# Performance work log

Hardware: AMD Instinct MI355X
Metric: run time of the kernel (lower is better)

## Reference

```python
import jax, jax.numpy as jnp
import numpy as np
import math

N_NODES = 50000
N_EDGES = 800000
IN_CH = 128
HID_CH = 16   # per-head channels of conv1
OUT_CH = 1    # per-head channels of conv2 (forced so Linear(heads,100) type-checks)
HEADS = 8


def _seg_softmax(scores, seg, n):
    # softmax over edges grouped by target node (variable-size neighborhoods)
    m = jax.ops.segment_max(scores, seg, num_segments=n)
    e = jnp.exp(scores - m[seg])
    s = jax.ops.segment_sum(e, seg, num_segments=n)
    return e / (s[seg] + 1e-16)


def _transformer_conv(x, edge_index, Wq, bq, Wk, bk, Wv, bv, Ws, bs, heads, ch):
    # PyG TransformerConv, concat=True, root_weight=True, beta=False
    n = x.shape[0]
    src, dst = edge_index[0], edge_index[1]
    q = (x @ Wq + bq).reshape(n, heads, ch)
    k = (x @ Wk + bk).reshape(n, heads, ch)
    v = (x @ Wv + bv).reshape(n, heads, ch)
    qi = q[dst]              # [E, H, C] gather at target
    kj = k[src]              # [E, H, C] gather at source
    vj = v[src]              # [E, H, C]
    alpha = jnp.einsum('ehc,ehc->eh', qi, kj) / math.sqrt(ch)  # [E, H]
    alpha = _seg_softmax(alpha, dst, n)
    agg = jax.ops.segment_sum(vj * alpha[:, :, None], dst, num_segments=n)
    out = agg.reshape(n, heads * ch)
    return out + x @ Ws + bs   # skip connection lin_skip(x)


def setup_inputs() -> dict:
    key = jax.random.key(0)
    ks = jax.random.split(key, 16)
    s = 0.05
    d1 = HEADS * HID_CH  # 128
    d2 = HEADS * OUT_CH  # 8
    inp = {
        'x': jax.random.normal(ks[0], (N_NODES, IN_CH), dtype=jnp.float32),
        'edge_index': jax.random.randint(ks[1], (2, N_EDGES), 0, N_NODES),
        # conv1 params
        'Wq1': jax.random.normal(ks[2], (IN_CH, d1), dtype=jnp.float32) * s,
        'bq1': jnp.zeros((d1,), jnp.float32),
        'Wk1': jax.random.normal(ks[3], (IN_CH, d1), dtype=jnp.float32) * s,
        'bk1': jnp.zeros((d1,), jnp.float32),
        'Wv1': jax.random.normal(ks[4], (IN_CH, d1), dtype=jnp.float32) * s,
        'bv1': jnp.zeros((d1,), jnp.float32),
        'Ws1': jax.random.normal(ks[5], (IN_CH, d1), dtype=jnp.float32) * s,
        'bs1': jnp.zeros((d1,), jnp.float32),
        # conv2 params (in = hidden*heads = 128)
        'Wq2': jax.random.normal(ks[6], (d1, d2), dtype=jnp.float32) * s,
        'bq2': jnp.zeros((d2,), jnp.float32),
        'Wk2': jax.random.normal(ks[7], (d1, d2), dtype=jnp.float32) * s,
        'bk2': jnp.zeros((d2,), jnp.float32),
        'Wv2': jax.random.normal(ks[8], (d1, d2), dtype=jnp.float32) * s,
        'bv2': jnp.zeros((d2,), jnp.float32),
        'Ws2': jax.random.normal(ks[9], (d1, d2), dtype=jnp.float32) * s,
        'bs2': jnp.zeros((d2,), jnp.float32),
        # final linear: heads -> 100
        'Wl': jax.random.normal(ks[10], (HEADS, 100), dtype=jnp.float32) * s,
        'bl': jnp.zeros((100,), jnp.float32),
    }
    return inp


def reference(x, edge_index, Wq1, bq1, Wk1, bk1, Wv1, bv1, Ws1, bs1,
              Wq2, bq2, Wk2, bk2, Wv2, bv2, Ws2, bs2, Wl, bl):
    h = _transformer_conv(x, edge_index, Wq1, bq1, Wk1, bk1, Wv1, bv1, Ws1, bs1, HEADS, HID_CH)
    h = _transformer_conv(h, edge_index, Wq2, bq2, Wk2, bk2, Wv2, bv2, Ws2, bs2, HEADS, OUT_CH)
    h = jax.nn.relu(h @ Wl + bl)   # dropout is identity in eval mode
    return jnp.mean(h, axis=0, keepdims=True)   # [1, 100]
```

## Files before the change

kernel.cpp:

```cpp
#include <hip/hip_runtime.h>
#include <hip/hip_bf16.h>
#include <cstdint>
#include <cstddef>


typedef _Float16 f16x8 __attribute__((ext_vector_type(8)));
typedef _Float16 f16x4 __attribute__((ext_vector_type(4)));
typedef _Float16 f16x2 __attribute__((ext_vector_type(2)));
typedef float    f32x4 __attribute__((ext_vector_type(4)));
typedef float    f32x2 __attribute__((ext_vector_type(2)));

#define SCAN_PAD 4096

__global__ __launch_bounds__(256) void pack_weights(
    const float* __restrict__ Wq1, const float* __restrict__ bq1,
    const float* __restrict__ Wk1, const float* __restrict__ bk1,
    const float* __restrict__ Wv1, const float* __restrict__ bv1,
    const float* __restrict__ Ws1, const float* __restrict__ bs1,
    const float* __restrict__ Wq2, const float* __restrict__ bq2,
    const float* __restrict__ Wk2, const float* __restrict__ bk2,
    const float* __restrict__ Wv2, const float* __restrict__ bv2,
    const float* __restrict__ Ws2, const float* __restrict__ bs2,
    _Float16* __restrict__ Wt1, float* __restrict__ b1,
    _Float16* __restrict__ Wt2, float* __restrict__ b2,
    int* __restrict__ counts, float* __restrict__ out, int n, int out_size)
{
    int i = blockIdx.x * 256 + threadIdx.x;
    if (i < n + SCAN_PAD) counts[i] = 0;
    if (i < out_size) out[i] = 0.f;
    if (i < 65536) {
        int j = i >> 7, k = i & 127;
        const float* W; int col; float sc = 1.f;
        if (j < 128)      { W = Wq1; col = j; sc = 0.25f; }
        else if (j < 384) { int t = j - 128, c = t >> 2, r = t & 3;
                            if (r < 2) { W = Wk1; col = 2 * c + r; }
                            else       { W = Wv1; col = 2 * c + r - 2; } }
        else              { W = Ws1; col = j - 384; }
        Wt1[i] = (_Float16)(W[k * 128 + col] * sc);
    } else if (i < 66048) {
        int j = i - 65536;
        const float* B; int col; float sc = 1.f;
        if (j < 128)      { B = bq1; col = j; sc = 0.25f; }
        else if (j < 384) { int t = j - 128, c = t >> 2, r = t & 3;
                            if (r < 2) { B = bk1; col = 2 * c + r; }
                            else       { B = bv1; col = 2 * c + r - 2; } }
        else              { B = bs1; col = j - 384; }
        b1[j] = B[col] * sc;
    } else if (i < 66048 + 4096) {
        int t = i - 66048;
        int j = t >> 7, k = t & 127;
        const float* W; int col;
        if (j < 8)       { W = Wq2; col = j; }
        else if (j < 24) { int u = j - 8; col = u >> 1; W = (u & 1) ? Wv2 : Wk2; }
        else             { W = Ws2; col = j - 24; }
        Wt2[t] = (_Float16)W[k * 8 + col];
    } else if (i < 66048 + 4096 + 32) {
        int j = i - (66048 + 4096);
        const float* B; int col;
        if (j < 8)       { B = bq2; col = j; }
        else if (j < 24) { int u = j - 8; col = u >> 1; B = (u & 1) ? bv2 : bk2; }
        else             { B = bs2; col = j - 24; }
        b2[j] = B[col];
    }
}

__global__ __launch_bounds__(256) void rank_edges(
    const int* __restrict__ ei, int* __restrict__ counts,
    unsigned short* __restrict__ rank, int E)
{
    int e0 = (blockIdx.x * 256 + threadIdx.x) * 4;
    if (e0 + 4 <= E) {
        int4 d4 = *(const int4*)&ei[E + e0];
        int r0 = atomicAdd(&counts[d4.x], 1);
        int r1 = atomicAdd(&counts[d4.y], 1);
        int r2 = atomicAdd(&counts[d4.z], 1);
        int r3 = atomicAdd(&counts[d4.w], 1);
        ushort4 rr = make_ushort4((unsigned short)r0, (unsigned short)r1,
                                  (unsigned short)r2, (unsigned short)r3);
        *(ushort4*)&rank[e0] = rr;
    } else {
        for (int e = e0; e < E; ++e)
            rank[e] = (unsigned short)atomicAdd(&counts[ei[E + e]], 1);
    }
}

__global__ __launch_bounds__(1024) void scan_all(
    const int* __restrict__ counts, int* __restrict__ indptr, int n, int E)
{
    int t = threadIdx.x, lane = t & 63;
    int lo = t * 52;
    int4 c[13];
    #pragma unroll
    for (int j = 0; j < 13; ++j) c[j] = *(const int4*)&counts[lo + j * 4];
    int s = 0;
    #pragma unroll
    for (int j = 0; j < 13; ++j) s += c[j].x + c[j].y + c[j].z + c[j].w;
    int x = s;
    #pragma unroll
    for (int off = 1; off < 64; off <<= 1) {
        int y = __shfl_up(x, off, 64);
        if (lane >= off) x += y;
    }
    __shared__ int ws[16];
    if (lane == 63) ws[t >> 6] = x;
    __syncthreads();
    int woff = 0;
    #pragma unroll
    for (int w = 0; w < 15; ++w) if (w < (t >> 6)) woff += ws[w];
    int run = woff + x - s;
    #pragma unroll
    for (int j = 0; j < 13; ++j) {
        int i = lo + j * 4;
        int4 v = c[j];
        int p0 = run, p1 = p0 + v.x, p2 = p1 + v.y, p3 = p2 + v.z;
        run = p3 + v.w;
        if (i + 3 < n) {
            *(int4*)&indptr[i] = make_int4(p0, p1, p2, p3);
        } else {
            if (i < n)     indptr[i]     = p0;
            if (i + 1 < n) indptr[i + 1] = p1;
            if (i + 2 < n) indptr[i + 2] = p2;
            if (i + 3 < n) indptr[i + 3] = p3;
        }
    }
    if (t == 0) indptr[n] = E;
}

__global__ __launch_bounds__(256) void place_edges(
    const int* __restrict__ ei, const int* __restrict__ indptr,
    const unsigned short* __restrict__ rank, unsigned short* __restrict__ srcs, int E)
{
    int e0 = (blockIdx.x * 256 + threadIdx.x) * 4;
    if (e0 + 4 <= E) {
        int4 s4 = *(const int4*)&ei[e0];
        int4 d4 = *(const int4*)&ei[E + e0];
        ushort4 r4 = *(const ushort4*)&rank[e0];
        srcs[indptr[d4.x] + r4.x] = (unsigned short)s4.x;
        srcs[indptr[d4.y] + r4.y] = (unsigned short)s4.y;
        srcs[indptr[d4.z] + r4.z] = (unsigned short)s4.z;
        srcs[indptr[d4.w] + r4.w] = (unsigned short)s4.w;
    } else {
        for (int e = e0; e < E; ++e)
            srcs[indptr[ei[E + e]] + rank[e]] = (unsigned short)ei[e];
    }
}

__global__ __launch_bounds__(256) void gemm1(
    const float* __restrict__ x, const _Float16* __restrict__ Wt1,
    const float* __restrict__ b1, _Float16* __restrict__ qs,
    unsigned char* __restrict__ kvbuf, int n)
{
    __shared__ _Float16 As[64][136];
    __shared__ _Float16 BD[64][136];
    int tid = threadIdx.x;
    int rowbase = blockIdx.x * 64;
    #pragma unroll
    for (int it = 0; it < 8; ++it) {
        int c = it * 256 + tid, row = c >> 5, ch = c & 31;
        float4 v = make_float4(0.f, 0.f, 0.f, 0.f);
        if (rowbase + row < n) v = *(const float4*)&x[(size_t)(rowbase + row) * 128 + ch * 4];
        f16x4 hv = { (_Float16)v.x, (_Float16)v.y, (_Float16)v.z, (_Float16)v.w };
        *(f16x4*)&As[row][ch * 4] = hv;
    }
    int w = tid >> 6, l = tid & 63;
    int wm = w >> 1, wn = w & 1, fr = l & 15, fg = l >> 4;
    for (int cb = 0; cb < 8; ++cb) {
        __syncthreads();
        #pragma unroll
        for (int it = 0; it < 4; ++it) {
            int c = it * 256 + tid, row = c >> 4, ch = c & 15;
            *(f16x8*)&BD[row][ch * 8] =
                *(const f16x8*)&Wt1[(size_t)(cb * 64 + row) * 128 + ch * 8];
        }
        __syncthreads();
        f32x4 acc[2][2] = {};
        #pragma unroll
        for (int kk = 0; kk < 4; ++kk) {
            int ko = kk * 32 + fg * 8;
            f16x8 a0 = *(const f16x8*)&As[wm * 32 + fr][ko];
            f16x8 a1 = *(const f16x8*)&As[wm * 32 + 16 + fr][ko];
            f16x8 b0 = *(const f16x8*)&BD[wn * 32 + fr][ko];
            f16x8 b1v = *(const f16x8*)&BD[wn * 32 + 16 + fr][ko];
            acc[0][0] = __builtin_amdgcn_mfma_f32_16x16x32_f16(a0, b0, acc[0][0], 0, 0, 0);
            acc[0][1] = __builtin_amdgcn_mfma_f32_16x16x32_f16(a0, b1v, acc[0][1], 0, 0, 0);
            acc[1][0] = __builtin_amdgcn_mfma_f32_16x16x32_f16(a1, b0, acc[1][0], 0, 0, 0);
            acc[1][1] = __builtin_amdgcn_mfma_f32_16x16x32_f16(a1, b1v, acc[1][1], 0, 0, 0);
        }
        __syncthreads();
        #pragma unroll
        for (int nt = 0; nt < 2; ++nt) {
            int col = wn * 32 + nt * 16 + fr;
            float bv = b1[cb * 64 + col];
            #pragma unroll
            for (int mt = 0; mt < 2; ++mt)
                #pragma unroll
                for (int r = 0; r < 4; ++r)
                    BD[wm * 32 + mt * 16 + fg * 4 + r][col] = (_Float16)(acc[mt][nt][r] + bv);
        }
        __syncthreads();
        if (cb >= 2 && cb < 6) {
            int row = tid >> 2, ch = tid & 3;
            if (rowbase + row < n) {
                f16x8 d0 = *(const f16x8*)&BD[row][ch * 16];
                f16x8 d1 = *(const f16x8*)&BD[row][ch * 16 + 8];
                int w0 = 0, w1 = 0, w2 = 0, w3 = 0;
                w0 = __builtin_amdgcn_cvt_pk_fp8_f32((float)d0[0], (float)d0[1], w0, false);
                w0 = __builtin_amdgcn_cvt_pk_fp8_f32((float)d0[2], (float)d0[3], w0, true);
                w1 = __builtin_amdgcn_cvt_pk_fp8_f32((float)d0[4], (float)d0[5], w1, false);
                w1 = __builtin_amdgcn_cvt_pk_fp8_f32((float)d0[6], (float)d0[7], w1, true);
                w2 = __builtin_amdgcn_cvt_pk_fp8_f32((float)d1[0], (float)d1[1], w2, false);
                w2 = __builtin_amdgcn_cvt_pk_fp8_f32((float)d1[2], (float)d1[3], w2, true);
                w3 = __builtin_amdgcn_cvt_pk_fp8_f32((float)d1[4], (float)d1[5], w3, false);
                w3 = __builtin_amdgcn_cvt_pk_fp8_f32((float)d1[6], (float)d1[7], w3, true);
                uint4 o = make_uint4((unsigned)w0, (unsigned)w1, (unsigned)w2, (unsigned)w3);
                *(uint4*)&kvbuf[(size_t)(rowbase + row) * 256 + (cb - 2) * 64 + ch * 16] = o;
            }
        } else {
            int dcol = (cb < 2) ? cb * 64 : (cb - 6) * 64 + 128;
            #pragma unroll
            for (int it = 0; it < 2; ++it) {
                int c = it * 256 + tid, row = c >> 3, ch = c & 7;
                if (rowbase + row < n)
                    *(f16x8*)&qs[(size_t)(rowbase + row) * 256 + dcol + ch * 8] =
                        *(const f16x8*)&BD[row][ch * 8];
            }
        }
    }
}

__global__ __launch_bounds__(256) void attn1(
    const _Float16* __restrict__ qs, const unsigned char* __restrict__ kvbuf,
    const int* __restrict__ indptr, const unsigned short* __restrict__ srcs,
    _Float16* __restrict__ h1, int n)
{
    int wid = threadIdx.x >> 6, l = threadIdx.x & 63;
    int node = blockIdx.x * 4 + wid;
    if (node >= n) return;
    int lam = l & 15, quarter = l >> 4;
    const _Float16* nrow = qs + (size_t)node * 256;
    f16x8 q8 = ((const f16x8*)nrow)[lam];
    float qf0 = (float)q8[0], qf1 = (float)q8[1], qf2 = (float)q8[2], qf3 = (float)q8[3];
    float qf4 = (float)q8[4], qf5 = (float)q8[5], qf6 = (float)q8[6], qf7 = (float)q8[7];
    float den = 0.f;
    float a0 = 0.f, a1 = 0.f, a2 = 0.f, a3 = 0.f;
    float a4 = 0.f, a5 = 0.f, a6 = 0.f, a7 = 0.f;
    int lane_off = lam * 16;

    auto edge = [&](uint4 kv, bool ok) {
        f32x2 k0 = __builtin_amdgcn_cvt_pk_f32_fp8((int)kv.x, false);
        f32x2 k1 = __builtin_amdgcn_cvt_pk_f32_fp8((int)kv.y, false);
        f32x2 k2 = __builtin_amdgcn_cvt_pk_f32_fp8((int)kv.z, false);
        f32x2 k3 = __builtin_amdgcn_cvt_pk_f32_fp8((int)kv.w, false);
        float p = k0.x * qf0 + k0.y * qf1 + k1.x * qf2 + k1.y * qf3
                + k2.x * qf4 + k2.y * qf5 + k3.x * qf6 + k3.y * qf7;
        p += __shfl_xor(p, 1, 64);
        float w = __expf(ok ? p : -1e30f);
        den += w;
        f32x2 v0 = __builtin_amdgcn_cvt_pk_f32_fp8((int)kv.x, true);
        f32x2 v1 = __builtin_amdgcn_cvt_pk_f32_fp8((int)kv.y, true);
        f32x2 v2 = __builtin_amdgcn_cvt_pk_f32_fp8((int)kv.z, true);
        f32x2 v3 = __builtin_amdgcn_cvt_pk_f32_fp8((int)kv.w, true);
        a0 = fmaf(w, v0.x, a0); a1 = fmaf(w, v0.y, a1);
        a2 = fmaf(w, v1.x, a2); a3 = fmaf(w, v1.y, a3);
        a4 = fmaf(w, v2.x, a4); a5 = fmaf(w, v2.y, a5);
        a6 = fmaf(w, v3.x, a6); a7 = fmaf(w, v3.y, a7);
    };

    int i0 = indptr[node], deg = indptr[node + 1] - i0;
    for (int base = 0; base < deg; base += 64) {
        int cnt = min(64, deg - base);
        int sv8 = 0;
        if (base + l < deg) sv8 = ((int)srcs[i0 + base + l]) << 8;
        int e = 0;
        for (; e + 8 <= cnt; e += 8) {
            int oA = __shfl(sv8, e + quarter, 64);
            int oB = __shfl(sv8, e + 4 + quarter, 64);
            uint4 kvA = *(const uint4*)(kvbuf + oA + lane_off);
            uint4 kvB = *(const uint4*)(kvbuf + oB + lane_off);
            edge(kvA, true); edge(kvB, true);
        }
        for (; e < cnt; e += 4) {
            int idx = e + quarter;
            int o = __shfl(sv8, idx, 64);
            uint4 kv = *(const uint4*)(kvbuf + o + lane_off);
            edge(kv, idx < cnt);
        }
    }
    den += __shfl_xor(den, 16, 64); den += __shfl_xor(den, 32, 64);
    a0 += __shfl_xor(a0, 16, 64); a0 += __shfl_xor(a0, 32, 64);
    a1 += __shfl_xor(a1, 16, 64); a1 += __shfl_xor(a1, 32, 64);
    a2 += __shfl_xor(a2, 16, 64); a2 += __shfl_xor(a2, 32, 64);
    a3 += __shfl_xor(a3, 16, 64); a3 += __shfl_xor(a3, 32, 64);
    a4 += __shfl_xor(a4, 16, 64); a4 += __shfl_xor(a4, 32, 64);
    a5 += __shfl_xor(a5, 16, 64); a5 += __shfl_xor(a5, 32, 64);
    a6 += __shfl_xor(a6, 16, 64); a6 += __shfl_xor(a6, 32, 64);
    a7 += __shfl_xor(a7, 16, 64); a7 += __shfl_xor(a7, 32, 64);
    if (quarter == 0) {
        float inv = 1.f / (den + 1e-16f);
        f16x8 s8 = ((const f16x8*)(nrow + 128))[lam];
        f16x8 o;
        o[0] = (_Float16)fmaf(a0, inv, (float)s8[0]);
        o[1] = (_Float16)fmaf(a1, inv, (float)s8[1]);
        o[2] = (_Float16)fmaf(a2, inv, (float)s8[2]);
        o[3] = (_Float16)fmaf(a3, inv, (float)s8[3]);
        o[4] = (_Float16)fmaf(a4, inv, (float)s8[4]);
        o[5] = (_Float16)fmaf(a5, inv, (float)s8[5]);
        o[6] = (_Float16)fmaf(a6, inv, (float)s8[6]);
        o[7] = (_Float16)fmaf(a7, inv, (float)s8[7]);
        ((f16x8*)(h1 + (size_t)node * 128))[lam] = o;
    }
}

__global__ __launch_bounds__(256) void gemm2(
    const _Float16* __restrict__ h1, const _Float16* __restrict__ Wt2,
    const float* __restrict__ b2, _Float16* __restrict__ qkvs2, int n)
{
    __shared__ _Float16 As[64][136];
    __shared__ _Float16 Bs[32][136];
    int tid = threadIdx.x;
    int rowbase = blockIdx.x * 64;
    #pragma unroll
    for (int it = 0; it < 4; ++it) {
        int c = it * 256 + tid, row = c >> 4, ch = c & 15;
        f16x8 v = {};
        if (rowbase + row < n) v = *(const f16x8*)&h1[(size_t)(rowbase + row) * 128 + ch * 8];
        *(f16x8*)&As[row][ch * 8] = v;
    }
    #pragma unroll
    for (int it = 0; it < 2; ++it) {
        int c = it * 256 + tid, row = c >> 4, ch = c & 15;
        *(f16x8*)&Bs[row][ch * 8] = *(const f16x8*)&Wt2[row * 128 + ch * 8];
    }
    __syncthreads();
    int w = tid >> 6, l = tid & 63, fr = l & 15, fg = l >> 4;
    f32x4 acc[2] = {};
    #pragma unroll
    for (int kk = 0; kk < 4; ++kk) {
        int ko = kk * 32 + fg * 8;
        f16x8 a = *(const f16x8*)&As[w * 16 + fr][ko];
        f16x8 b0 = *(const f16x8*)&Bs[fr][ko];
        f16x8 b1v = *(const f16x8*)&Bs[16 + fr][ko];
        acc[0] = __builtin_amdgcn_mfma_f32_16x16x32_f16(a, b0, acc[0], 0, 0, 0);
        acc[1] = __builtin_amdgcn_mfma_f32_16x16x32_f16(a, b1v, acc[1], 0, 0, 0);
    }
    #pragma unroll
    for (int nt = 0; nt < 2; ++nt) {
        int col = nt * 16 + fr;
        float bv = b2[col];
        #pragma unroll
        for (int r = 0; r < 4; ++r) {
            int row = rowbase + w * 16 + fg * 4 + r;
            if (row < n) qkvs2[(size_t)row * 32 + col] = (_Float16)(acc[nt][r] + bv);
        }
    }
}

__global__ __launch_bounds__(256) void attn2(
    const _Float16* __restrict__ q2, const int* __restrict__ indptr,
    const unsigned short* __restrict__ srcs, float* __restrict__ h2, int n)
{
    int wid = threadIdx.x >> 6, l = threadIdx.x & 63;
    int node = blockIdx.x * 4 + wid;
    if (node >= n) return;
    int i = l >> 3, h = l & 7;
    const _Float16* base = q2 + (size_t)node * 32;
    float qh = (float)base[h];
    int i0 = indptr[node], i1 = indptr[node + 1];
    float den = 0.f, acc = 0.f;
    for (int p = i0 + i; p < i1; p += 8) {
        int s = srcs[p];
        f16x2 kv = ((const f16x2*)(q2 + (size_t)s * 32 + 8))[h];
        float w = __expf(qh * (float)kv.x);
        den += w;
        acc = fmaf(w, (float)kv.y, acc);
    }
    den += __shfl_xor(den, 8, 64); den += __shfl_xor(den, 16, 64); den += __shfl_xor(den, 32, 64);
    acc += __shfl_xor(acc, 8, 64); acc += __shfl_xor(acc, 16, 64); acc += __shfl_xor(acc, 32, 64);
    if (i == 0)
        h2[(size_t)node * 8 + h] = acc / (den + 1e-16f) + (float)base[24 + h];
}

__global__ __launch_bounds__(128) void final_reduce(
    const float* __restrict__ h2, const float* __restrict__ Wl,
    const float* __restrict__ bl, float* __restrict__ out, int n, int chunk)
{
    int j = threadIdx.x;
    bool act = j < 100;
    float wl[8] = {};
    float bj = 0.f;
    if (act) {
        #pragma unroll
        for (int t = 0; t < 8; ++t) wl[t] = Wl[t * 100 + j];
        bj = bl[j];
    }
    int lo = blockIdx.x * chunk, hi = min(n, lo + chunk);
    float acc = 0.f;
    for (int node = lo; node < hi; ++node) {
        const float* hr = h2 + (size_t)node * 8;
        float y = bj;
        #pragma unroll
        for (int t = 0; t < 8; ++t) y += hr[t] * wl[t];
        acc += fmaxf(y, 0.f);
    }
    if (act) atomicAdd(&out[j], acc * (1.f / (float)n));
}

extern "C" void kernel_launch(void* const* d_in, const int* in_sizes, int n_in,
                              void* d_out, int out_size, void* d_ws, size_t ws_size,
                              hipStream_t stream)
{
    const float* x   = (const float*)d_in[0];
    const int*   ei  = (const int*)d_in[1];
    const float* Wq1 = (const float*)d_in[2],  *bq1 = (const float*)d_in[3];
    const float* Wk1 = (const float*)d_in[4],  *bk1 = (const float*)d_in[5];
    const float* Wv1 = (const float*)d_in[6],  *bv1 = (const float*)d_in[7];
    const float* Ws1 = (const float*)d_in[8],  *bs1 = (const float*)d_in[9];
    const float* Wq2 = (const float*)d_in[10], *bq2 = (const float*)d_in[11];
    const float* Wk2 = (const float*)d_in[12], *bk2 = (const float*)d_in[13];
    const float* Wv2 = (const float*)d_in[14], *bv2 = (const float*)d_in[15];
    const float* Ws2 = (const float*)d_in[16], *bs2 = (const float*)d_in[17];
    const float* Wl  = (const float*)d_in[18], *bl  = (const float*)d_in[19];
    float* out = (float*)d_out;

    int n = in_sizes[0] / 128;
    int E = in_sizes[1] / 2;

    char* p = (char*)d_ws;
    auto take = [&](size_t bytes) -> void* {
        void* r = (void*)p;
        p += (bytes + 255) & ~(size_t)255;
        return r;
    };
    _Float16*       qs     = (_Float16*)take((size_t)n * 256 * 2);
    unsigned char*  kvbuf  = (unsigned char*)take((size_t)n * 256);
    _Float16*       h1     = (_Float16*)take((size_t)n * 128 * 2);
    _Float16*       qkvs2  = (_Float16*)take((size_t)n * 32 * 2);
    float*          h2     = (float*)take((size_t)n * 8 * 4);
    _Float16*       Wt1    = (_Float16*)take(65536 * 2);
    float*          b1     = (float*)take(512 * 4);
    _Float16*       Wt2    = (_Float16*)take(4096 * 2);
    float*          b2     = (float*)take(32 * 4);
    int*            counts = (int*)take((size_t)(n + SCAN_PAD) * 4);
    int*            indptr = (int*)take((size_t)(n + 1) * 4);
    unsigned short* rank   = (unsigned short*)take((size_t)E * 2);
    unsigned short* srcs   = (unsigned short*)take((size_t)E * 2);

    pack_weights<<<(70400 + 255) / 256, 256, 0, stream>>>(
        Wq1, bq1, Wk1, bk1, Wv1, bv1, Ws1, bs1,
        Wq2, bq2, Wk2, bk2, Wv2, bv2, Ws2, bs2,
        Wt1, b1, Wt2, b2, counts, out, n, out_size);

    int eb = (E / 4 + 255) / 256;
    rank_edges<<<eb, 256, 0, stream>>>(ei, counts, rank, E);
    scan_all<<<1, 1024, 0, stream>>>(counts, indptr, n, E);
    place_edges<<<eb, 256, 0, stream>>>(ei, indptr, rank, srcs, E);

    gemm1<<<(n + 63) / 64, 256, 0, stream>>>(x, Wt1, b1, qs, kvbuf, n);
    attn1<<<(n + 3) / 4, 256, 0, stream>>>(qs, kvbuf, indptr, srcs, h1, n);
    gemm2<<<(n + 63) / 64, 256, 0, stream>>>(h1, Wt2, b2, qkvs2, n);
    attn2<<<(n + 3) / 4, 256, 0, stream>>>(qkvs2, indptr, srcs, h2, n);

    int chunk = (n + 255) / 256;
    final_reduce<<<256, 128, 0, stream>>>(h2, Wl, bl, out, n, chunk);
}
```

Before: 283.8 us.

## Fuse CSR build into cooperative kernel and fold gemm2 into attn1

Merges the three CSR construction kernels (ranking atomics, scan, placement) into one cooperative kernel that uses grid syncs and keeps ranks in registers, which removes the rank buffer and two launches. It also fuses the layer-2 projection into the layer-1 attention kernel. Each wave writes its node's hidden row to shared memory and computes the 32 outputs with scalar FMAs against weights staged in shared memory, so the h1 round-trip and the gemm2 launch go away. The costs are that every attention block reloads Wt2 into shared memory, the MFMA GEMM is replaced by scalar FMAs, and the cooperative launch requires all 196 blocks of 1024 threads to be co-resident.

New measurement: 360.8 us. +27.1%, slower.

```diff
diff --git a/kernel.cpp b/kernel.cpp
--- a/kernel.cpp
+++ b/kernel.cpp
@@ -1,7 +1,10 @@
 #include <hip/hip_runtime.h>
 #include <hip/hip_bf16.h>
+#include <hip/hip_cooperative_groups.h>
 #include <cstdint>
 #include <cstddef>
+
+namespace cg = cooperative_groups;
 
 
 typedef _Float16 f16x8 __attribute__((ext_vector_type(8)));
@@ -64,84 +67,78 @@
     }
 }
 
-__global__ __launch_bounds__(256) void rank_edges(
+__global__ __launch_bounds__(1024) void build_csr(
     const int* __restrict__ ei, int* __restrict__ counts,
-    unsigned short* __restrict__ rank, int E)
-{
-    int e0 = (blockIdx.x * 256 + threadIdx.x) * 4;
-    if (e0 + 4 <= E) {
-        int4 d4 = *(const int4*)&ei[E + e0];
-        int r0 = atomicAdd(&counts[d4.x], 1);
-        int r1 = atomicAdd(&counts[d4.y], 1);
-        int r2 = atomicAdd(&counts[d4.z], 1);
-        int r3 = atomicAdd(&counts[d4.w], 1);
-        ushort4 rr = make_ushort4((unsigned short)r0, (unsigned short)r1,
-                                  (unsigned short)r2, (unsigned short)r3);
-        *(ushort4*)&rank[e0] = rr;
-    } else {
-        for (int e = e0; e < E; ++e)
-            rank[e] = (unsigned short)atomicAdd(&counts[ei[E + e]], 1);
-    }
-}
-
-__global__ __launch_bounds__(1024) void scan_all(
-    const int* __restrict__ counts, int* __restrict__ indptr, int n, int E)
-{
-    int t = threadIdx.x, lane = t & 63;
-    int lo = t * 52;
-    int4 c[13];
-    #pragma unroll
-    for (int j = 0; j < 13; ++j) c[j] = *(const int4*)&counts[lo + j * 4];
-    int s = 0;
-    #pragma unroll
-    for (int j = 0; j < 13; ++j) s += c[j].x + c[j].y + c[j].z + c[j].w;
-    int x = s;
-    #pragma unroll
-    for (int off = 1; off < 64; off <<= 1) {
-        int y = __shfl_up(x, off, 64);
-        if (lane >= off) x += y;
-    }
-    __shared__ int ws[16];
-    if (lane == 63) ws[t >> 6] = x;
-    __syncthreads();
-    int woff = 0;
-    #pragma unroll
-    for (int w = 0; w < 15; ++w) if (w < (t >> 6)) woff += ws[w];
-    int run = woff + x - s;
-    #pragma unroll
-    for (int j = 0; j < 13; ++j) {
-        int i = lo + j * 4;
-        int4 v = c[j];
-        int p0 = run, p1 = p0 + v.x, p2 = p1 + v.y, p3 = p2 + v.z;
-        run = p3 + v.w;
-        if (i + 3 < n) {
-            *(int4*)&indptr[i] = make_int4(p0, p1, p2, p3);
-        } else {
-            if (i < n)     indptr[i]     = p0;
-            if (i + 1 < n) indptr[i + 1] = p1;
-            if (i + 2 < n) indptr[i + 2] = p2;
-            if (i + 3 < n) indptr[i + 3] = p3;
-        }
-    }
-    if (t == 0) indptr[n] = E;
-}
-
-__global__ __launch_bounds__(256) void place_edges(
-    const int* __restrict__ ei, const int* __restrict__ indptr,
-    const unsigned short* __restrict__ rank, unsigned short* __restrict__ srcs, int E)
-{
-    int e0 = (blockIdx.x * 256 + threadIdx.x) * 4;
-    if (e0 + 4 <= E) {
-        int4 s4 = *(const int4*)&ei[e0];
-        int4 d4 = *(const int4*)&ei[E + e0];
-        ushort4 r4 = *(const ushort4*)&rank[e0];
-        srcs[indptr[d4.x] + r4.x] = (unsigned short)s4.x;
-        srcs[indptr[d4.y] + r4.y] = (unsigned short)s4.y;
-        srcs[indptr[d4.z] + r4.z] = (unsigned short)s4.z;
-        srcs[indptr[d4.w] + r4.w] = (unsigned short)s4.w;
-    } else {
-        for (int e = e0; e < E; ++e)
-            srcs[indptr[ei[E + e]] + rank[e]] = (unsigned short)ei[e];
+    int* __restrict__ indptr, unsigned short* __restrict__ srcs, int E, int n)
+{
+    cg::grid_group grid = cg::this_grid();
+    int gtid = blockIdx.x * 1024 + threadIdx.x;
+    int e0 = gtid * 4;
+    int cnt = E - e0;
+    int4 d4 = make_int4(0, 0, 0, 0), s4 = make_int4(0, 0, 0, 0);
+    int r0 = 0, r1 = 0, r2 = 0, r3 = 0;
+    if (cnt >= 4) {
+        d4 = *(const int4*)&ei[E + e0];
+        s4 = *(const int4*)&ei[e0];
+        r0 = atomicAdd(&counts[d4.x], 1);
+        r1 = atomicAdd(&counts[d4.y], 1);
+        r2 = atomicAdd(&counts[d4.z], 1);
+        r3 = atomicAdd(&counts[d4.w], 1);
+    } else if (cnt > 0) {
+        { s4.x = ei[e0];     d4.x = ei[E + e0];     r0 = atomicAdd(&counts[d4.x], 1); }
+        if (cnt > 1) { s4.y = ei[e0 + 1]; d4.y = ei[E + e0 + 1]; r1 = atomicAdd(&counts[d4.y], 1); }
+        if (cnt > 2) { s4.z = ei[e0 + 2]; d4.z = ei[E + e0 + 2]; r2 = atomicAdd(&counts[d4.z], 1); }
+    }
+    grid.sync();
+    if (blockIdx.x == 0) {
+        int t = threadIdx.x, lane = t & 63;
+        int lo = t * 52;
+        int4 c[13];
+        #pragma unroll
+        for (int j = 0; j < 13; ++j) c[j] = *(const int4*)&counts[lo + j * 4];
+        int s = 0;
+        #pragma unroll
+        for (int j = 0; j < 13; ++j) s += c[j].x + c[j].y + c[j].z + c[j].w;
+        int x = s;
+        #pragma unroll
+        for (int off = 1; off < 64; off <<= 1) {
+            int y = __shfl_up(x, off, 64);
+            if (lane >= off) x += y;
+        }
+        __shared__ int ws[16];
+        if (lane == 63) ws[t >> 6] = x;
+        __syncthreads();
+        int woff = 0;
+        #pragma unroll
+        for (int w = 0; w < 15; ++w) if (w < (t >> 6)) woff += ws[w];
+        int run = woff + x - s;
+        #pragma unroll
+        for (int j = 0; j < 13; ++j) {
+            int i = lo + j * 4;
+            int4 v = c[j];
+            int p0 = run, p1 = p0 + v.x, p2 = p1 + v.y, p3 = p2 + v.z;
+            run = p3 + v.w;
+            if (i + 3 < n) {
+                *(int4*)&indptr[i] = make_int4(p0, p1, p2, p3);
+            } else {
+                if (i < n)     indptr[i]     = p0;
+                if (i + 1 < n) indptr[i + 1] = p1;
+                if (i + 2 < n) indptr[i + 2] = p2;
+                if (i + 3 < n) indptr[i + 3] = p3;
+            }
+        }
+        if (t == 0) indptr[n] = E;
+    }
+    grid.sync();
+    if (cnt >= 4) {
+        srcs[indptr[d4.x] + r0] = (unsigned short)s4.x;
+        srcs[indptr[d4.y] + r1] = (unsigned short)s4.y;
+        srcs[indptr[d4.z] + r2] = (unsigned short)s4.z;
+        srcs[indptr[d4.w] + r3] = (unsigned short)s4.w;
+    } else if (cnt > 0) {
+        srcs[indptr[d4.x] + r0] = (unsigned short)s4.x;
+        if (cnt > 1) srcs[indptr[d4.y] + r1] = (unsigned short)s4.y;
+        if (cnt > 2) srcs[indptr[d4.z] + r2] = (unsigned short)s4.z;
     }
 }
 
@@ -228,12 +225,22 @@
     }
 }
 
-__global__ __launch_bounds__(256) void attn1(
+__global__ __launch_bounds__(256) void attn1_fused(
     const _Float16* __restrict__ qs, const unsigned char* __restrict__ kvbuf,
     const int* __restrict__ indptr, const unsigned short* __restrict__ srcs,
-    _Float16* __restrict__ h1, int n)
-{
-    int wid = threadIdx.x >> 6, l = threadIdx.x & 63;
+    const _Float16* __restrict__ Wt2, const float* __restrict__ b2,
+    _Float16* __restrict__ qkvs2, int n)
+{
+    __shared__ _Float16 Wt2s[32][136];
+    __shared__ _Float16 h1s[4][136];
+    int tid = threadIdx.x;
+    #pragma unroll
+    for (int it = 0; it < 2; ++it) {
+        int c = it * 256 + tid, row = c >> 4, ch = c & 15;
+        *(f16x8*)&Wt2s[row][ch * 8] = *(const f16x8*)&Wt2[row * 128 + ch * 8];
+    }
+    __syncthreads();
+    int wid = tid >> 6, l = tid & 63;
     int node = blockIdx.x * 4 + wid;
     if (node >= n) return;
     int lam = l & 15, quarter = l >> 4;
@@ -295,64 +302,31 @@
     a5 += __shfl_xor(a5, 16, 64); a5 += __shfl_xor(a5, 32, 64);
     a6 += __shfl_xor(a6, 16, 64); a6 += __shfl_xor(a6, 32, 64);
     a7 += __shfl_xor(a7, 16, 64); a7 += __shfl_xor(a7, 32, 64);
+    float inv = 1.f / (den + 1e-16f);
+    f16x8 s8 = ((const f16x8*)(nrow + 128))[lam];
     if (quarter == 0) {
-        float inv = 1.f / (den + 1e-16f);
-        f16x8 s8 = ((const f16x8*)(nrow + 128))[lam];
-        f16x8 o;
-        o[0] = (_Float16)fmaf(a0, inv, (float)s8[0]);
-        o[1] = (_Float16)fmaf(a1, inv, (float)s8[1]);
-        o[2] = (_Float16)fmaf(a2, inv, (float)s8[2]);
-        o[3] = (_Float16)fmaf(a3, inv, (float)s8[3]);
-        o[4] = (_Float16)fmaf(a4, inv, (float)s8[4]);
-        o[5] = (_Float16)fmaf(a5, inv, (float)s8[5]);
-        o[6] = (_Float16)fmaf(a6, inv, (float)s8[6]);
-        o[7] = (_Float16)fmaf(a7, inv, (float)s8[7]);
-        ((f16x8*)(h1 + (size_t)node * 128))[lam] = o;
-    }
-}
-
-__global__ __launch_bounds__(256) void gemm2(
-    const _Float16* __restrict__ h1, const _Float16* __restrict__ Wt2,
-    const float* __restrict__ b2, _Float16* __restrict__ qkvs2, int n)
-{
-    __shared__ _Float16 As[64][136];
-    __shared__ _Float16 Bs[32][136];
-    int tid = threadIdx.x;
-    int rowbase = blockIdx.x * 64;
+        f16x8 hh;
+        hh[0] = (_Float16)fmaf(a0, inv, (float)s8[0]);
+        hh[1] = (_Float16)fmaf(a1, inv, (float)s8[1]);
+        hh[2] = (_Float16)fmaf(a2, inv, (float)s8[2]);
+        hh[3] = (_Float16)fmaf(a3, inv, (float)s8[3]);
+        hh[4] = (_Float16)fmaf(a4, inv, (float)s8[4]);
+        hh[5] = (_Float16)fmaf(a5, inv, (float)s8[5]);
+        hh[6] = (_Float16)fmaf(a6, inv, (float)s8[6]);
+        hh[7] = (_Float16)fmaf(a7, inv, (float)s8[7]);
+        *(f16x8*)&h1s[wid][lam * 8] = hh;
+    }
+    int j = l & 31, hf = l >> 5;
+    float acc2 = 0.f;
     #pragma unroll
-    for (int it = 0; it < 4; ++it) {
-        int c = it * 256 + tid, row = c >> 4, ch = c & 15;
-        f16x8 v = {};
-        if (rowbase + row < n) v = *(const f16x8*)&h1[(size_t)(rowbase + row) * 128 + ch * 8];
-        *(f16x8*)&As[row][ch * 8] = v;
-    }
-    #pragma unroll
-    for (int it = 0; it < 2; ++it) {
-        int c = it * 256 + tid, row = c >> 4, ch = c & 15;
-        *(f16x8*)&Bs[row][ch * 8] = *(const f16x8*)&Wt2[row * 128 + ch * 8];
-    }
-    __syncthreads();
-    int w = tid >> 6, l = tid & 63, fr = l & 15, fg = l >> 4;
-    f32x4 acc[2] = {};
-    #pragma unroll
-    for (int kk = 0; kk < 4; ++kk) {
-        int ko = kk * 32 + fg * 8;
-        f16x8 a = *(const f16x8*)&As[w * 16 + fr][ko];
-        f16x8 b0 = *(const f16x8*)&Bs[fr][ko];
-        f16x8 b1v = *(const f16x8*)&Bs[16 + fr][ko];
-        acc[0] = __builtin_amdgcn_mfma_f32_16x16x32_f16(a, b0, acc[0], 0, 0, 0);
-        acc[1] = __builtin_amdgcn_mfma_f32_16x16x32_f16(a, b1v, acc[1], 0, 0, 0);
-    }
-    #pragma unroll
-    for (int nt = 0; nt < 2; ++nt) {
-        int col = nt * 16 + fr;
-        float bv = b2[col];
-        #pragma unroll
-        for (int r = 0; r < 4; ++r) {
-            int row = rowbase + w * 16 + fg * 4 + r;
-            if (row < n) qkvs2[(size_t)row * 32 + col] = (_Float16)(acc[nt][r] + bv);
-        }
-    }
+    for (int c8 = 0; c8 < 8; ++c8) {
+        f16x8 hv = *(const f16x8*)&h1s[wid][hf * 64 + c8 * 8];
+        f16x8 wv = *(const f16x8*)&Wt2s[j][hf * 64 + c8 * 8];
+        #pragma unroll
+        for (int t = 0; t < 8; ++t) acc2 = fmaf((float)hv[t], (float)wv[t], acc2);
+    }
+    acc2 += __shfl_xor(acc2, 32, 64);
+    if (l < 32) qkvs2[(size_t)node * 32 + j] = (_Float16)(acc2 + b2[j]);
 }
 
 __global__ __launch_bounds__(256) void attn2(
@@ -433,7 +407,6 @@
     };
     _Float16*       qs     = (_Float16*)take((size_t)n * 256 * 2);
     unsigned char*  kvbuf  = (unsigned char*)take((size_t)n * 256);
-    _Float16*       h1     = (_Float16*)take((size_t)n * 128 * 2);
     _Float16*       qkvs2  = (_Float16*)take((size_t)n * 32 * 2);
     float*          h2     = (float*)take((size_t)n * 8 * 4);
     _Float16*       Wt1    = (_Float16*)take(65536 * 2);
@@ -442,7 +415,6 @@
     float*          b2     = (float*)take(32 * 4);
     int*            counts = (int*)take((size_t)(n + SCAN_PAD) * 4);
     int*            indptr = (int*)take((size_t)(n + 1) * 4);
-    unsigned short* rank   = (unsigned short*)take((size_t)E * 2);
     unsigned short* srcs   = (unsigned short*)take((size_t)E * 2);
 
     pack_weights<<<(70400 + 255) / 256, 256, 0, stream>>>(
@@ -450,14 +422,16 @@
         Wq2, bq2, Wk2, bk2, Wv2, bv2, Ws2, bs2,
         Wt1, b1, Wt2, b2, counts, out, n, out_size);
 
-    int eb = (E / 4 + 255) / 256;
-    rank_edges<<<eb, 256, 0, stream>>>(ei, counts, rank, E);
-    scan_all<<<1, 1024, 0, stream>>>(counts, indptr, n, E);
-    place_edges<<<eb, 256, 0, stream>>>(ei, indptr, rank, srcs, E);
+    {
+        int nbc = (E + 4095) / 4096;
+        void* args[] = { (void*)&ei, (void*)&counts, (void*)&indptr,
+                         (void*)&srcs, (void*)&E, (void*)&n };
+        hipLaunchCooperativeKernel((const void*)build_csr, dim3(nbc), dim3(1024),
+                                   args, 0, stream);
+    }
 
     gemm1<<<(n + 63) / 64, 256, 0, stream>>>(x, Wt1, b1, qs, kvbuf, n);
-    attn1<<<(n + 3) / 4, 256, 0, stream>>>(qs, kvbuf, indptr, srcs, h1, n);
-    gemm2<<<(n + 63) / 64, 256, 0, stream>>>(h1, Wt2, b2, qkvs2, n);
+    attn1_fused<<<(n + 3) / 4, 256, 0, stream>>>(qs, kvbuf, indptr, srcs, Wt2, b2, qkvs2, n);
     attn2<<<(n + 3) / 4, 256, 0, stream>>>(qkvs2, indptr, srcs, h2, n);
 
     int chunk = (n + 255) / 256;
```
